# Kernel tuning notes

Hardware: AMD Instinct MI355X
Metric: run time of the kernel (lower is better)

## Reference

```python
import jax, jax.numpy as jnp
import numpy as np

NEG_SLOPE = 0.2

def _smlp(x, w, b):
    # torch nn.Linear convention: y = x @ w.T + b, then leaky_relu(0.2)
    return jax.nn.leaky_relu(x @ w.T + b, NEG_SLOPE)

_gather = jax.vmap(lambda a, i: a[i])  # (N,C),(N,k) -> (N,k,C), vmapped over batch

def _lfa(points, feats, idx, w, b):
    # points: (B,N,3), feats: (B,N,F_D), idx: (B,N,k)
    knn_p = _gather(points, idx)                      # (B,N,k,3)
    rel = points[:, :, None, :] - knn_p               # (B,N,k,3)
    dist = jnp.linalg.norm(rel, axis=-1, keepdims=True)
    geo = jnp.concatenate([rel, dist], axis=-1)       # (B,N,k,4)
    mlp = _smlp(geo, w, b)                            # (B,N,k,d)
    knn_f = _gather(feats, idx)                       # (B,N,k,F_D)
    return jnp.concatenate([mlp, knn_f], axis=-1).mean(axis=2)  # (B,N,d+F_D)

def setup_inputs() -> dict:
    key = jax.random.key(0)
    ks = jax.random.split(key, 12)
    B, N, K, D = 2, 65536, 32, 64
    pts = jax.random.normal(ks[0], (B, N, 3), jnp.float32)
    feats = jax.random.normal(ks[1], (B, N, D), jnp.float32)
    idx = jax.random.randint(ks[2], (B, N, K), 0, N)
    def lin(k, o, i):
        bound = 1.0 / np.sqrt(i)
        kw, kb = jax.random.split(k)
        return (jax.random.uniform(kw, (o, i), jnp.float32, -bound, bound),
                jax.random.uniform(kb, (o,), jnp.float32, -bound, bound))
    w_init, b_init = lin(ks[3], D // 4, D)
    w_lfa1, b_lfa1 = lin(ks[4], D // 4, 4)
    w_lfa2, b_lfa2 = lin(ks[5], D // 2, 4)
    w_final, b_final = lin(ks[6], D, D)
    w_res, b_res = lin(ks[7], D, D)
    return {"points": pts, "features": feats, "knn_indices": idx,
            "w_init": w_init, "b_init": b_init,
            "w_lfa1": w_lfa1, "b_lfa1": b_lfa1,
            "w_lfa2": w_lfa2, "b_lfa2": b_lfa2,
            "w_final": w_final, "b_final": b_final,
            "w_res": w_res, "b_res": b_res}

def reference(points, features, knn_indices, w_init, b_init,
              w_lfa1, b_lfa1, w_lfa2, b_lfa2,
              w_final, b_final, w_res, b_res):
    x = _smlp(features, w_init, b_init)               # (B,N,16)
    x = _lfa(points, x, knn_indices, w_lfa1, b_lfa1)  # (B,N,32)
    x = _lfa(points, x, knn_indices, w_lfa2, b_lfa2)  # (B,N,64)
    x = _smlp(x, w_final, b_final)                    # (B,N,64)
    residual = _smlp(features, w_res, b_res)          # (B,N,64)
    return x + residual
```

## Files before the change

### kernel.cpp

```cpp
#include <hip/hip_runtime.h>
#include <math.h>

#define NPTS 65536

typedef unsigned short ushort_t;
typedef unsigned int uint_t;
typedef __attribute__((ext_vector_type(8))) short bf16x8;
typedef __attribute__((ext_vector_type(4))) float f32x4;
typedef __attribute__((ext_vector_type(2))) float f32x2;

__device__ __forceinline__ float lrelu(float x) {
  return fmaxf(x, 0.2f * x);
}
__device__ __forceinline__ f32x2 lrelu2(f32x2 s) {
  return __builtin_elementwise_max(s, s * 0.2f);
}
__device__ __forceinline__ ushort_t f2b(float f) {
  union { float f; uint_t u; } v; v.f = f;
  uint_t u = v.u + (0x7fffu + ((v.u >> 16) & 1u));
  return (ushort_t)(u >> 16);
}
__device__ __forceinline__ float b2f_lo(uint_t u) {
  union { uint_t u; float f; } v; v.u = u << 16; return v.f;
}
__device__ __forceinline__ float b2f_hi(uint_t u) {
  union { uint_t u; float f; } v; v.u = u & 0xffff0000u; return v.f;
}
__device__ __forceinline__ bf16x8 cvt8(const float* p) {
  float4 a = ((const float4*)p)[0];
  float4 b = ((const float4*)p)[1];
  float f[8] = {a.x, a.y, a.z, a.w, b.x, b.y, b.z, b.w};
  bf16x8 r;
#pragma unroll
  for (int j = 0; j < 8; ++j) r[j] = (short)f2b(f[j]);
  return r;
}

__device__ __forceinline__ int swz_pbase(int ppb) {
  int bid = blockIdx.x;
  if ((int)gridDim.x * ppb == 2 * NPTS) {
    int g = bid >> 3, x = bid & 7;
    return (x >> 2) * NPTS + (g * 4 + (x & 3)) * ppb;
  }
  return bid * ppb;
}

__global__ __launch_bounds__(256) void k_init(
    const float* __restrict__ feats, const float* __restrict__ w,
    const float* __restrict__ bia, ushort_t* __restrict__ x1,
    const float* __restrict__ pts, float4* __restrict__ pts4,
    const float* __restrict__ wf, const float* __restrict__ wr,
    ushort_t* __restrict__ wfb, ushort_t* __restrict__ wrb, int BN) {
  __shared__ float wt[64 * 16];
  int t = threadIdx.x;
  if (blockIdx.x < 2) {
    const float* src = blockIdx.x ? wr : wf;
    ushort_t* dst = blockIdx.x ? wrb : wfb;
    for (int e = t; e < 4096; e += 256) dst[e] = f2b(src[e]);
  }
  for (int e = t; e < 1024; e += 256) {
    int o = e >> 6, i = e & 63;
    wt[i * 16 + o] = w[e];
  }
  __syncthreads();
  int p = blockIdx.x * 256 + t;
  if (p >= BN) return;
  const float* pp = pts + (size_t)p * 3;
  pts4[p] = make_float4(pp[0], pp[1], pp[2], 0.0f);
  float acc[16];
#pragma unroll
  for (int o = 0; o < 16; ++o) acc[o] = bia[o];
  const float4* xr4 = (const float4*)(feats + (size_t)p * 64);
#pragma unroll 4
  for (int i4 = 0; i4 < 16; ++i4) {
    float4 xv = xr4[i4];
    float xs[4] = {xv.x, xv.y, xv.z, xv.w};
#pragma unroll
    for (int s = 0; s < 4; ++s) {
      float xi = xs[s];
      const float4* w4 = (const float4*)&wt[(i4 * 4 + s) * 16];
#pragma unroll
      for (int q = 0; q < 4; ++q) {
        float4 wv = w4[q];
        acc[q * 4 + 0] = fmaf(xi, wv.x, acc[q * 4 + 0]);
        acc[q * 4 + 1] = fmaf(xi, wv.y, acc[q * 4 + 1]);
        acc[q * 4 + 2] = fmaf(xi, wv.z, acc[q * 4 + 2]);
        acc[q * 4 + 3] = fmaf(xi, wv.w, acc[q * 4 + 3]);
      }
    }
  }
  union { ushort_t u[16]; uint4 v[2]; } pk;
#pragma unroll
  for (int o = 0; o < 16; ++o) pk.u[o] = f2b(lrelu(acc[o]));
  uint4* op = (uint4*)(x1 + (size_t)p * 16);
  op[0] = pk.v[0];
  op[1] = pk.v[1];
}

__global__ __launch_bounds__(256) void k_lfa1g(
    const float4* __restrict__ pts4, const ushort_t* __restrict__ fin,
    const int* __restrict__ idx, const float* __restrict__ w1,
    const float* __restrict__ b1, const float* __restrict__ w2,
    const float* __restrict__ b2, ushort_t* __restrict__ x2out,
    ushort_t* __restrict__ g2out, int BN) {
  int t = threadIdx.x;
  int p = swz_pbase(32) + (t >> 3);
  int sub = t & 7;
  if (p >= BN) return;
  int base = p & ~(NPTS - 1);
  float4 mp = pts4[p];
  const float* w1b = w1 + sub * 8;
  f32x2 w1p[4], b1p;
#pragma unroll
  for (int k = 0; k < 4; ++k) w1p[k] = f32x2{w1b[k], w1b[4 + k]};
  b1p = f32x2{b1[sub * 2], b1[sub * 2 + 1]};
  const float* w2b = w2 + sub * 16;
  f32x2 w2p[2][4], b2p[2];
#pragma unroll
  for (int pr = 0; pr < 2; ++pr) {
#pragma unroll
    for (int k = 0; k < 4; ++k)
      w2p[pr][k] = f32x2{w2b[pr * 8 + k], w2b[pr * 8 + 4 + k]};
    b2p[pr] = f32x2{b2[sub * 4 + pr * 2], b2[sub * 4 + pr * 2 + 1]};
  }
  f32x2 m1 = {0.f, 0.f}, f1 = {0.f, 0.f};
  f32x2 m2[2] = {{0.f, 0.f}, {0.f, 0.f}};
  const int4* iv4 = (const int4*)(idx + (size_t)p * 32);
#pragma unroll 2
  for (int kk = 0; kk < 8; ++kk) {
    int4 iv = iv4[kk];
    int js[4] = {iv.x, iv.y, iv.z, iv.w};
#pragma unroll
    for (int u = 0; u < 4; ++u) {
      int j = base + js[u];
      float4 pj = pts4[j];
      uint_t fv = *((const uint_t*)(fin + (size_t)j * 16) + sub);
      float rx = mp.x - pj.x, ry = mp.y - pj.y, rz = mp.z - pj.z;
      float d = sqrtf(fmaf(rx, rx, fmaf(ry, ry, rz * rz)));
      f32x2 vx = {rx, rx}, vy = {ry, ry}, vz = {rz, rz}, vd = {d, d};
      f32x2 s = __builtin_elementwise_fma(vd, w1p[3], b1p);
      s = __builtin_elementwise_fma(vz, w1p[2], s);
      s = __builtin_elementwise_fma(vy, w1p[1], s);
      s = __builtin_elementwise_fma(vx, w1p[0], s);
      m1 += lrelu2(s);
#pragma unroll
      for (int pr = 0; pr < 2; ++pr) {
        f32x2 s2 = __builtin_elementwise_fma(vd, w2p[pr][3], b2p[pr]);
        s2 = __builtin_elementwise_fma(vz, w2p[pr][2], s2);
        s2 = __builtin_elementwise_fma(vy, w2p[pr][1], s2);
        s2 = __builtin_elementwise_fma(vx, w2p[pr][0], s2);
        m2[pr] += lrelu2(s2);
      }
      f1 += f32x2{b2f_lo(fv), b2f_hi(fv)};
    }
  }
  const float inv = 1.0f / 32.0f;
  ushort_t* orow = x2out + (size_t)p * 32;
  union { ushort_t u[2]; uint_t v; } pm, pf;
  pm.u[0] = f2b(m1.x * inv); pm.u[1] = f2b(m1.y * inv);
  pf.u[0] = f2b(f1.x * inv); pf.u[1] = f2b(f1.y * inv);
  ((uint_t*)orow)[sub] = pm.v;
  ((uint_t*)orow)[8 + sub] = pf.v;
  union { ushort_t u[4]; uint2 v; } pg;
  pg.u[0] = f2b(m2[0].x * inv); pg.u[1] = f2b(m2[0].y * inv);
  pg.u[2] = f2b(m2[1].x * inv); pg.u[3] = f2b(m2[1].y * inv);
  ((uint2*)(g2out + (size_t)p * 32))[sub] = pg.v;
}

__global__ __launch_bounds__(256) void k_lfa2f(
    const ushort_t* __restrict__ fin, const int* __restrict__ idx,
    const ushort_t* __restrict__ g2, const float* __restrict__ feats,
    const ushort_t* __restrict__ wfb, const float* __restrict__ bfi,
    const ushort_t* __restrict__ wrb, const float* __restrict__ bri,
    float* __restrict__ out, int BN) {
  int t = threadIdx.x;
  int lane = t & 63, wave = t >> 6;
  int n = lane & 15, quad = lane >> 4;
  int wbase = swz_pbase(64) + wave * 16;
  int p0 = wbase + n;
  int p = p0 < BN ? p0 : BN - 1;
  int base = p & ~(NPTS - 1);
  f32x2 fa[4];
#pragma unroll
  for (int o = 0; o < 4; ++o) fa[o] = f32x2{0.f, 0.f};
  const int4* iv4 = (const int4*)(idx + (size_t)p * 32);
#pragma unroll 8
  for (int kk = 0; kk < 8; ++kk) {
    int4 iv = iv4[kk];
    int js[4] = {iv.x, iv.y, iv.z, iv.w};
#pragma unroll
    for (int u = 0; u < 4; ++u) {
      int j = base + js[u];
      uint4 fv = *((const uint4*)(fin + (size_t)j * 32) + quad);
      fa[0] += f32x2{b2f_lo(fv.x), b2f_hi(fv.x)};
      fa[1] += f32x2{b2f_lo(fv.y), b2f_hi(fv.y)};
      fa[2] += f32x2{b2f_lo(fv.z), b2f_hi(fv.z)};
      fa[3] += f32x2{b2f_lo(fv.w), b2f_hi(fv.w)};
    }
  }
  const float inv = 1.0f / 32.0f;
  bf16x8 Ax0 = *((const bf16x8*)(g2 + (size_t)p * 32 + quad * 8));
  bf16x8 Ax1;
#pragma unroll
  for (int o = 0; o < 4; ++o) {
    Ax1[o * 2 + 0] = (short)f2b(fa[o].x * inv);
    Ax1[o * 2 + 1] = (short)f2b(fa[o].y * inv);
  }
  const float* af = feats + (size_t)p * 64 + quad * 8;
  bf16x8 Af0 = cvt8(af), Af1 = cvt8(af + 32);
  float y[16];
#pragma unroll
  for (int nt = 0; nt < 4; ++nt) {
    f32x4 acc = {0.f, 0.f, 0.f, 0.f};
    int woff = (nt * 16 + n) * 64 + quad * 8;
    bf16x8 Bf0 = *((const bf16x8*)(wfb + woff));
    bf16x8 Bf1 = *((const bf16x8*)(wfb + woff + 32));
    acc = __builtin_amdgcn_mfma_f32_16x16x32_bf16(Ax0, Bf0, acc, 0, 0, 0);
    acc = __builtin_amdgcn_mfma_f32_16x16x32_bf16(Ax1, Bf1, acc, 0, 0, 0);
    float bv = bfi[nt * 16 + n];
#pragma unroll
    for (int r = 0; r < 4; ++r) y[nt * 4 + r] = lrelu(acc[r] + bv);
  }
#pragma unroll
  for (int nt = 0; nt < 4; ++nt) {
    f32x4 acc = {0.f, 0.f, 0.f, 0.f};
    int woff = (nt * 16 + n) * 64 + quad * 8;
    bf16x8 Br0 = *((const bf16x8*)(wrb + woff));
    bf16x8 Br1 = *((const bf16x8*)(wrb + woff + 32));
    acc = __builtin_amdgcn_mfma_f32_16x16x32_bf16(Af0, Br0, acc, 0, 0, 0);
    acc = __builtin_amdgcn_mfma_f32_16x16x32_bf16(Af1, Br1, acc, 0, 0, 0);
    float bv = bri[nt * 16 + n];
#pragma unroll
    for (int r = 0; r < 4; ++r) {
      int row = wbase + quad * 4 + r;
      if (row < BN) out[(size_t)row * 64 + nt * 16 + n] = y[nt * 4 + r] + lrelu(acc[r] + bv);
    }
  }
}

extern "C" void kernel_launch(void* const* d_in, const int* in_sizes, int n_in,
                              void* d_out, int out_size, void* d_ws, size_t ws_size,
                              hipStream_t stream) {
  const float* pts    = (const float*)d_in[0];
  const float* feats  = (const float*)d_in[1];
  const int*   idx    = (const int*)d_in[2];
  const float* w_init = (const float*)d_in[3];
  const float* b_init = (const float*)d_in[4];
  const float* w_l1   = (const float*)d_in[5];
  const float* b_l1   = (const float*)d_in[6];
  const float* w_l2   = (const float*)d_in[7];
  const float* b_l2   = (const float*)d_in[8];
  const float* w_f    = (const float*)d_in[9];
  const float* b_f    = (const float*)d_in[10];
  const float* w_r    = (const float*)d_in[11];
  const float* b_r    = (const float*)d_in[12];
  float* out = (float*)d_out;

  int BN = in_sizes[2] / 32;
  ushort_t* x1 = (ushort_t*)d_ws;
  ushort_t* x2 = x1 + (size_t)BN * 16;
  float4* pts4 = (float4*)(x2 + (size_t)BN * 32);
  ushort_t* wfb = (ushort_t*)(pts4 + BN);
  ushort_t* wrb = wfb + 4096;
  ushort_t* g2 = wrb + 4096;

  int blocks_pt = (BN + 255) / 256;
  int blocks_l1 = (BN + 31) / 32;
  int blocks_l2 = (BN + 63) / 64;

  k_init<<<blocks_pt, 256, 0, stream>>>(feats, w_init, b_init, x1, pts, pts4,
                                        w_f, w_r, wfb, wrb, BN);
  k_lfa1g<<<blocks_l1, 256, 0, stream>>>(pts4, x1, idx, w_l1, b_l1, w_l2, b_l2,
                                         x2, g2, BN);
  k_lfa2f<<<blocks_l2, 256, 0, stream>>>(x2, idx, g2, feats, wfb, b_f, wrb, b_r,
                                         out, BN);
}
```

Measured before the change: 233.0 us.

## Tune occupancy hints, use raw v_sqrt, unroll more, and merge MFMA epilogue loops

Adds launch-bound occupancy hints to both LFA kernels and raises the unroll factor of the neighbour loop in the first LFA kernel. Replaces sqrtf with an inline-asm v_sqrt_f32 to skip the IEEE-correct sqrt expansion. Merges the two MFMA loops in the final kernel so each output tile computes both the final and the residual projection together, removing the 16-float y buffer and lowering register pressure. The occupancy hints can force register spilling, and the raw sqrt is slightly less accurate.

```diff
diff --git a/kernel.cpp b/kernel.cpp
--- a/kernel.cpp
+++ b/kernel.cpp
@@ -14,6 +14,11 @@
 }
 __device__ __forceinline__ f32x2 lrelu2(f32x2 s) {
   return __builtin_elementwise_max(s, s * 0.2f);
+}
+__device__ __forceinline__ float fast_sqrtf(float x) {
+  float r;
+  asm("v_sqrt_f32 %0, %1" : "=v"(r) : "v"(x));
+  return r;
 }
 __device__ __forceinline__ ushort_t f2b(float f) {
   union { float f; uint_t u; } v; v.f = f;
@@ -97,7 +102,7 @@
   op[1] = pk.v[1];
 }
 
-__global__ __launch_bounds__(256) void k_lfa1g(
+__global__ __launch_bounds__(256, 8) void k_lfa1g(
     const float4* __restrict__ pts4, const ushort_t* __restrict__ fin,
     const int* __restrict__ idx, const float* __restrict__ w1,
     const float* __restrict__ b1, const float* __restrict__ w2,
@@ -126,7 +131,7 @@
   f32x2 m1 = {0.f, 0.f}, f1 = {0.f, 0.f};
   f32x2 m2[2] = {{0.f, 0.f}, {0.f, 0.f}};
   const int4* iv4 = (const int4*)(idx + (size_t)p * 32);
-#pragma unroll 2
+#pragma unroll 4
   for (int kk = 0; kk < 8; ++kk) {
     int4 iv = iv4[kk];
     int js[4] = {iv.x, iv.y, iv.z, iv.w};
@@ -136,7 +141,7 @@
       float4 pj = pts4[j];
       uint_t fv = *((const uint_t*)(fin + (size_t)j * 16) + sub);
       float rx = mp.x - pj.x, ry = mp.y - pj.y, rz = mp.z - pj.z;
-      float d = sqrtf(fmaf(rx, rx, fmaf(ry, ry, rz * rz)));
+      float d = fast_sqrtf(fmaf(rx, rx, fmaf(ry, ry, rz * rz)));
       f32x2 vx = {rx, rx}, vy = {ry, ry}, vz = {rz, rz}, vd = {d, d};
       f32x2 s = __builtin_elementwise_fma(vd, w1p[3], b1p);
       s = __builtin_elementwise_fma(vz, w1p[2], s);
@@ -167,7 +172,7 @@
   ((uint2*)(g2out + (size_t)p * 32))[sub] = pg.v;
 }
 
-__global__ __launch_bounds__(256) void k_lfa2f(
+__global__ __launch_bounds__(256, 6) void k_lfa2f(
     const ushort_t* __restrict__ fin, const int* __restrict__ idx,
     const ushort_t* __restrict__ g2, const float* __restrict__ feats,
     const ushort_t* __restrict__ wfb, const float* __restrict__ bfi,
@@ -208,32 +213,27 @@
   }
   const float* af = feats + (size_t)p * 64 + quad * 8;
   bf16x8 Af0 = cvt8(af), Af1 = cvt8(af + 32);
-  float y[16];
 #pragma unroll
   for (int nt = 0; nt < 4; ++nt) {
-    f32x4 acc = {0.f, 0.f, 0.f, 0.f};
     int woff = (nt * 16 + n) * 64 + quad * 8;
     bf16x8 Bf0 = *((const bf16x8*)(wfb + woff));
     bf16x8 Bf1 = *((const bf16x8*)(wfb + woff + 32));
-    acc = __builtin_amdgcn_mfma_f32_16x16x32_bf16(Ax0, Bf0, acc, 0, 0, 0);
-    acc = __builtin_amdgcn_mfma_f32_16x16x32_bf16(Ax1, Bf1, acc, 0, 0, 0);
-    float bv = bfi[nt * 16 + n];
-#pragma unroll
-    for (int r = 0; r < 4; ++r) y[nt * 4 + r] = lrelu(acc[r] + bv);
-  }
-#pragma unroll
-  for (int nt = 0; nt < 4; ++nt) {
-    f32x4 acc = {0.f, 0.f, 0.f, 0.f};
-    int woff = (nt * 16 + n) * 64 + quad * 8;
+    f32x4 accx = {0.f, 0.f, 0.f, 0.f};
+    accx = __builtin_amdgcn_mfma_f32_16x16x32_bf16(Ax0, Bf0, accx, 0, 0, 0);
+    accx = __builtin_amdgcn_mfma_f32_16x16x32_bf16(Ax1, Bf1, accx, 0, 0, 0);
     bf16x8 Br0 = *((const bf16x8*)(wrb + woff));
     bf16x8 Br1 = *((const bf16x8*)(wrb + woff + 32));
-    acc = __builtin_amdgcn_mfma_f32_16x16x32_bf16(Af0, Br0, acc, 0, 0, 0);
-    acc = __builtin_amdgcn_mfma_f32_16x16x32_bf16(Af1, Br1, acc, 0, 0, 0);
-    float bv = bri[nt * 16 + n];
+    f32x4 accr = {0.f, 0.f, 0.f, 0.f};
+    accr = __builtin_amdgcn_mfma_f32_16x16x32_bf16(Af0, Br0, accr, 0, 0, 0);
+    accr = __builtin_amdgcn_mfma_f32_16x16x32_bf16(Af1, Br1, accr, 0, 0, 0);
+    float bvf = bfi[nt * 16 + n];
+    float bvr = bri[nt * 16 + n];
 #pragma unroll
     for (int r = 0; r < 4; ++r) {
       int row = wbase + quad * 4 + r;
-      if (row < BN) out[(size_t)row * 64 + nt * 16 + n] = y[nt * 4 + r] + lrelu(acc[r] + bv);
+      if (row < BN)
+        out[(size_t)row * 64 + nt * 16 + n] =
+            lrelu(accx[r] + bvf) + lrelu(accr[r] + bvr);
     }
   }
 }
```

After: 423.9 us. +81.9%, slower.
